# Kernel optimization log

Hardware: AMD Instinct MI355X
Metric: run time of the kernel (lower is better)

The kernel has to match this reference:

```python
import jax, jax.numpy as jnp
import numpy as np

B, C, F, H, W = 4, 256, 16, 32, 32


def setup_inputs() -> dict:
    key = jax.random.key(0)
    ks = jax.random.split(key, 8)
    x = jax.random.normal(ks[0], (B, C, F, H, W), dtype=jnp.float32)
    wq = jax.random.normal(ks[1], (C, C), dtype=jnp.float32) * 0.05
    bq = jax.random.normal(ks[2], (C,), dtype=jnp.float32) * 0.05
    wk = jax.random.normal(ks[3], (C, C), dtype=jnp.float32) * 0.05
    bk = jax.random.normal(ks[4], (C,), dtype=jnp.float32) * 0.05
    wv = jax.random.normal(ks[5], (C, C), dtype=jnp.float32) * 0.05
    bv = jax.random.normal(ks[6], (C,), dtype=jnp.float32) * 0.05
    gamma = jax.random.normal(ks[7], (1,), dtype=jnp.float32) * 0.1
    return {"x": x, "wq": wq, "bq": bq, "wk": wk, "bk": bk, "wv": wv, "bv": bv, "gamma": gamma}


def reference(x, wq, bq, wk, bk, wv, bv, gamma):
    b, c, f, h, w = x.shape
    p = h * w
    # replicate torch .view(batch*frames, channels, H, W): raw memory reinterpretation
    xr = x.reshape(b * f, c, p)  # [B*F, C, HW]
    proj = lambda wt, bi: jnp.einsum('ncp,dc->ndp', xr, wt) + bi[None, :, None]
    q = proj(wq, bq).reshape(b, f, c, p).transpose(0, 2, 1, 3)  # [B, C, F, HW]
    k = proj(wk, bk).reshape(b, f, c, p).transpose(0, 2, 3, 1)  # [B, C, HW, F]
    v = proj(wv, bv).reshape(b, f, c, p).transpose(0, 2, 1, 3)  # [B, C, F, HW]
    attn = jax.nn.softmax(jnp.matmul(q, k) * (1.0 / c ** 0.5), axis=-1)  # [B, C, F, F]
    out = jnp.matmul(attn, v)  # [B, C, F, HW]
    # replicate permute(0,2,1,3).view(B,F,C,H,W).permute(0,2,1,3,4)
    out = out.transpose(0, 2, 1, 3).reshape(b, f, c, h, w).transpose(0, 2, 1, 3, 4)
    return gamma * out + x
```

## Files before the change

kernel.cpp:

```cpp
#include <hip/hip_runtime.h>
#include <hip/hip_bf16.h>

#define CC 256
#define FF 16
#define PP 1024
#define BB 4
#define NN 64

typedef __bf16 bf16x8 __attribute__((ext_vector_type(8)));
typedef float  f32x4  __attribute__((ext_vector_type(4)));

__device__ __forceinline__ void async16(const __hip_bfloat16* g, char* l) {
    __builtin_amdgcn_global_load_lds(
        (const __attribute__((address_space(1))) unsigned int*)g,
        (__attribute__((address_space(3))) unsigned int*)l, 16, 0, 0);
}

__global__ __launch_bounds__(256) void xt_kernel(
    const float* __restrict__ x, __hip_bfloat16* __restrict__ Xt)
{
    __shared__ float T[64][65];
    const int n = blockIdx.z, c0 = blockIdx.y * 64, p0 = blockIdx.x * 64;
    const int t = threadIdx.x;
    const int pl = t & 63, r0 = t >> 6;
    const float* xp = x + ((size_t)n * CC + c0) * PP + p0;
    #pragma unroll
    for (int i = 0; i < 16; ++i) {
        const int cl = r0 + i * 4;
        T[cl][pl] = xp[(size_t)cl * PP + pl];
    }
    __syncthreads();
    __hip_bfloat16* op = Xt + ((size_t)n * PP + p0) * CC + c0;
    const int cl2 = (t & 31) * 2, q0 = t >> 5;
    #pragma unroll
    for (int j = 0; j < 8; ++j) {
        const int pr = q0 + j * 8;
        __hip_bfloat162 h;
        h.x = __float2bfloat16(T[cl2][pr]);
        h.y = __float2bfloat16(T[cl2 + 1][pr]);
        *(__hip_bfloat162*)(op + (size_t)pr * CC + cl2) = h;
    }
}

__global__ __launch_bounds__(256) void wconv_kernel(
    const float* __restrict__ wq, const float* __restrict__ wk,
    const float* __restrict__ wv, __hip_bfloat16* __restrict__ Wb)
{
    const int proj = blockIdx.y;
    const float* src = proj == 0 ? wq : (proj == 1 ? wk : wv);
    __hip_bfloat16* dst = Wb + (size_t)proj * CC * CC;
    const int idx = (blockIdx.x * 256 + threadIdx.x) * 4;
    const float4 v = *(const float4*)(src + idx);
    dst[idx + 0] = __float2bfloat16(v.x);
    dst[idx + 1] = __float2bfloat16(v.y);
    dst[idx + 2] = __float2bfloat16(v.z);
    dst[idx + 3] = __float2bfloat16(v.w);
}

__global__ __launch_bounds__(256) void qkv_mfma(
    const __hip_bfloat16* __restrict__ Wb, const __hip_bfloat16* __restrict__ Xt,
    const float* __restrict__ bq, const float* __restrict__ bk,
    const float* __restrict__ bv,
    __hip_bfloat16* __restrict__ Qw, __hip_bfloat16* __restrict__ Kw,
    float* __restrict__ Vout)
{
    __shared__ char lds[36864];

    const int p0 = blockIdx.x * 128, d0 = blockIdx.y * 128;
    const int z = blockIdx.z, proj = z % 3, n = z / 3;
    const int t = threadIdx.x, w = t >> 6, lane = t & 63;
    const int wd = (w >> 1) * 64, wp = (w & 1) * 64;
    const int q = lane >> 4, m16 = lane & 15;

    const __hip_bfloat16* Abase = Wb + (size_t)proj * CC * CC + (size_t)d0 * CC;
    const __hip_bfloat16* Bbase = Xt + (size_t)n * PP * CC + (size_t)p0 * CC;

    f32x4 acc[4][4];
    #pragma unroll
    for (int i = 0; i < 4; ++i)
        #pragma unroll
        for (int j = 0; j < 4; ++j)
            acc[i][j] = (f32x4){0.f, 0.f, 0.f, 0.f};

    for (int c0 = 0; c0 < CC; c0 += 64) {
        #pragma unroll
        for (int k = 0; k < 4; ++k) {
            const int s = t + 256 * k;
            const int row = s >> 3;
            const int gc = (s & 7) ^ (row & 7);
            async16(Abase + (size_t)row * CC + c0 + gc * 8, lds + s * 16);
            async16(Bbase + (size_t)row * CC + c0 + gc * 8, lds + 16384 + s * 16);
        }
        __syncthreads();
        #pragma unroll
        for (int kk = 0; kk < 2; ++kk) {
            bf16x8 a[4], b[4];
            #pragma unroll
            for (int i = 0; i < 4; ++i) {
                const int row = wd + i * 16 + m16;
                const int col = (4 * kk + q) ^ (row & 7);
                a[i] = *(const bf16x8*)(lds + row * 128 + col * 16);
            }
            #pragma unroll
            for (int j = 0; j < 4; ++j) {
                const int row = wp + j * 16 + m16;
                const int col = (4 * kk + q) ^ (row & 7);
                b[j] = *(const bf16x8*)(lds + 16384 + row * 128 + col * 16);
            }
            #pragma unroll
            for (int i = 0; i < 4; ++i)
                #pragma unroll
                for (int j = 0; j < 4; ++j)
                    acc[i][j] = __builtin_amdgcn_mfma_f32_16x16x32_bf16(a[i], b[j], acc[i][j], 0, 0, 0);
        }
        __syncthreads();
    }

    __syncthreads();
    char* wb = lds + w * 9216;
    const int dl2 = lane >> 3, pl2 = lane & 7;

    if (proj < 2) {
        const float* bias = (proj == 0) ? bq : bk;
        #pragma unroll
        for (int i = 0; i < 4; ++i)
            #pragma unroll
            for (int r = 0; r < 4; ++r) {
                const int d_l = i * 16 + q * 4 + r;
                const float bb = bias[d0 + wd + d_l];
                #pragma unroll
                for (int j = 0; j < 4; ++j) {
                    const int p_l = j * 16 + m16;
                    *(__hip_bfloat16*)(wb + d_l * 144 + p_l * 2) =
                        __float2bfloat16(acc[i][j][r] + bb);
                }
            }
        __hip_bfloat16* dst = ((proj == 0) ? Qw : Kw) + (size_t)n * CC * PP;
        #pragma unroll
        for (int k = 0; k < 8; ++k) {
            const int d_l = k * 8 + dl2;
            bf16x8 v = *(const bf16x8*)(wb + d_l * 144 + pl2 * 16);
            *(bf16x8*)(dst + (size_t)(d0 + wd + d_l) * PP + p0 + wp + pl2 * 8) = v;
        }
    } else {
        const int b = n >> 4, f = n & 15;
        #pragma unroll
        for (int h = 0; h < 2; ++h) {
            #pragma unroll
            for (int i = 0; i < 4; ++i)
                #pragma unroll
                for (int r = 0; r < 4; ++r) {
                    const int d_l = i * 16 + q * 4 + r;
                    const float bb = bv[d0 + wd + d_l];
                    #pragma unroll
                    for (int jj = 0; jj < 2; ++jj) {
                        const int j = 2 * h + jj;
                        const int p_rel = jj * 16 + m16;
                        *(float*)(wb + d_l * 144 + p_rel * 4) = acc[i][j][r] + bb;
                    }
                }
            #pragma unroll
            for (int k = 0; k < 8; ++k) {
                const int d_l = k * 8 + dl2;
                f32x4 v = *(const f32x4*)(wb + d_l * 144 + pl2 * 16);
                const int p = p0 + wp + h * 32 + pl2 * 4;
                *(f32x4*)(Vout + (((size_t)(b * CC + d0 + wd + d_l)) * FF + f) * PP + p) = v;
            }
        }
    }
}

__global__ __launch_bounds__(256) void attn_out(
    const __hip_bfloat16* __restrict__ Qw, const __hip_bfloat16* __restrict__ Kw,
    const float* __restrict__ x, const float* __restrict__ gamma,
    float* __restrict__ out)
{
    const int d = blockIdx.x, b = blockIdx.y;
    const int t = threadIdx.x, w = t >> 6, lane = t & 63;
    const int q = lane >> 4, m16 = lane & 15;
    __shared__ float Sp[4][16][17];
    __shared__ float As[16][17];

    {
        const size_t gbase = ((size_t)(b * 16 + m16) * CC + d) * PP + w * 256 + q * 8;
        f32x4 acc0 = {0.f, 0.f, 0.f, 0.f}, acc1 = {0.f, 0.f, 0.f, 0.f};
        #pragma unroll
        for (int pc = 0; pc < 256; pc += 64) {
            bf16x8 aq0 = *(const bf16x8*)(Qw + gbase + pc);
            bf16x8 bk0 = *(const bf16x8*)(Kw + gbase + pc);
            bf16x8 aq1 = *(const bf16x8*)(Qw + gbase + pc + 32);
            bf16x8 bk1 = *(const bf16x8*)(Kw + gbase + pc + 32);
            acc0 = __builtin_amdgcn_mfma_f32_16x16x32_bf16(aq0, bk0, acc0, 0, 0, 0);
            acc1 = __builtin_amdgcn_mfma_f32_16x16x32_bf16(aq1, bk1, acc1, 0, 0, 0);
        }
        #pragma unroll
        for (int r = 0; r < 4; ++r)
            Sp[w][q * 4 + r][m16] = acc0[r] + acc1[r];
    }
    __syncthreads();

    {
        const int f1 = t >> 4, f2 = t & 15;
        const float s = (Sp[0][f1][f2] + Sp[1][f1][f2] + Sp[2][f1][f2] + Sp[3][f1][f2]) * 0.0625f;
        float m = s;
        #pragma unroll
        for (int off = 1; off < 16; off <<= 1) m = fmaxf(m, __shfl_xor(m, off));
        const float e = __expf(s - m);
        float den = e;
        #pragma unroll
        for (int off = 1; off < 16; off <<= 1) den += __shfl_xor(den, off);
        As[f1][f2] = e / den;
    }
    __syncthreads();

    const float g = gamma[0];
    const size_t base = ((size_t)(b * CC + d) * FF) * PP + t * 4;
    f32x4 vv[16];
    #pragma unroll
    for (int f2 = 0; f2 < 16; ++f2)
        vv[f2] = *(const f32x4*)(out + base + (size_t)f2 * PP);
    #pragma unroll
    for (int f1 = 0; f1 < 16; ++f1) {
        f32x4 a = {0.f, 0.f, 0.f, 0.f};
        #pragma unroll
        for (int f2 = 0; f2 < 16; ++f2) {
            const float av = As[f1][f2];
            a += av * vv[f2];
        }
        const f32x4 xv = *(const f32x4*)(x + base + (size_t)f1 * PP);
        const f32x4 res = g * a + xv;
        *(f32x4*)(out + base + (size_t)f1 * PP) = res;
    }
}

extern "C" void kernel_launch(void* const* d_in, const int* in_sizes, int n_in,
                              void* d_out, int out_size, void* d_ws, size_t ws_size,
                              hipStream_t stream) {
    const float* x     = (const float*)d_in[0];
    const float* wq    = (const float*)d_in[1];
    const float* bq    = (const float*)d_in[2];
    const float* wk    = (const float*)d_in[3];
    const float* bk    = (const float*)d_in[4];
    const float* wv    = (const float*)d_in[5];
    const float* bv    = (const float*)d_in[6];
    const float* gamma = (const float*)d_in[7];
    float* out = (float*)d_out;

    __hip_bfloat16* Qw = (__hip_bfloat16*)d_ws;
    __hip_bfloat16* Kw = Qw + (size_t)NN * CC * PP;
    __hip_bfloat16* Xt = Kw + (size_t)NN * CC * PP;
    __hip_bfloat16* Wb = Xt + (size_t)NN * CC * PP;

    wconv_kernel<<<dim3(CC * CC / (256 * 4), 3), 256, 0, stream>>>(wq, wk, wv, Wb);
    xt_kernel<<<dim3(PP / 64, CC / 64, NN), 256, 0, stream>>>(x, Xt);
    qkv_mfma<<<dim3(PP / 128, CC / 128, NN * 3), 256, 0, stream>>>(
        Wb, Xt, bq, bk, bv, Qw, Kw, out);
    attn_out<<<dim3(CC, BB), 256, 0, stream>>>(Qw, Kw, x, gamma, out);
}
```

Baseline: 200.7 us.

## Store V in bf16 workspace, fuse weight conversion into transpose kernel

V projection output is written as bf16 to a dedicated workspace buffer instead of fp32 into the output tensor, and attn_out reads and widens it. This halves V write and read traffic. The weight-conversion kernel is folded into xt_kernel as an extra z-slice, removing one launch. Xt is now staged in the output buffer. Storing V in bf16 adds rounding error to the attention output.

```diff
diff --git a/kernel.cpp b/kernel.cpp
--- a/kernel.cpp
+++ b/kernel.cpp
@@ -16,12 +16,38 @@
         (__attribute__((address_space(3))) unsigned int*)l, 16, 0, 0);
 }
 
+__device__ __forceinline__ float bf2f(unsigned short u) {
+    union { unsigned i; float f; } v; v.i = ((unsigned)u) << 16; return v.f;
+}
+
 __global__ __launch_bounds__(256) void xt_kernel(
-    const float* __restrict__ x, __hip_bfloat16* __restrict__ Xt)
+    const float* __restrict__ x,
+    const float* __restrict__ wq, const float* __restrict__ wk,
+    const float* __restrict__ wv,
+    __hip_bfloat16* __restrict__ Xt, __hip_bfloat16* __restrict__ Wb)
 {
     __shared__ float T[64][65];
-    const int n = blockIdx.z, c0 = blockIdx.y * 64, p0 = blockIdx.x * 64;
+    const int n = blockIdx.z;
     const int t = threadIdx.x;
+
+    if (n == NN) {
+        const int blk = blockIdx.y * 16 + blockIdx.x;
+        const int idx = (blk * 256 + t) * 4;
+        #pragma unroll
+        for (int proj = 0; proj < 3; ++proj) {
+            const float* src = proj == 0 ? wq : (proj == 1 ? wk : wv);
+            __hip_bfloat16* dst = Wb + (size_t)proj * CC * CC;
+            const float4 v = *(const float4*)(src + idx);
+            __hip_bfloat162 h0, h1;
+            h0.x = __float2bfloat16(v.x); h0.y = __float2bfloat16(v.y);
+            h1.x = __float2bfloat16(v.z); h1.y = __float2bfloat16(v.w);
+            *(__hip_bfloat162*)(dst + idx)     = h0;
+            *(__hip_bfloat162*)(dst + idx + 2) = h1;
+        }
+        return;
+    }
+
+    const int c0 = blockIdx.y * 64, p0 = blockIdx.x * 64;
     const int pl = t & 63, r0 = t >> 6;
     const float* xp = x + ((size_t)n * CC + c0) * PP + p0;
     #pragma unroll
@@ -42,27 +68,12 @@
     }
 }
 
-__global__ __launch_bounds__(256) void wconv_kernel(
-    const float* __restrict__ wq, const float* __restrict__ wk,
-    const float* __restrict__ wv, __hip_bfloat16* __restrict__ Wb)
-{
-    const int proj = blockIdx.y;
-    const float* src = proj == 0 ? wq : (proj == 1 ? wk : wv);
-    __hip_bfloat16* dst = Wb + (size_t)proj * CC * CC;
-    const int idx = (blockIdx.x * 256 + threadIdx.x) * 4;
-    const float4 v = *(const float4*)(src + idx);
-    dst[idx + 0] = __float2bfloat16(v.x);
-    dst[idx + 1] = __float2bfloat16(v.y);
-    dst[idx + 2] = __float2bfloat16(v.z);
-    dst[idx + 3] = __float2bfloat16(v.w);
-}
-
 __global__ __launch_bounds__(256) void qkv_mfma(
     const __hip_bfloat16* __restrict__ Wb, const __hip_bfloat16* __restrict__ Xt,
     const float* __restrict__ bq, const float* __restrict__ bk,
     const float* __restrict__ bv,
     __hip_bfloat16* __restrict__ Qw, __hip_bfloat16* __restrict__ Kw,
-    float* __restrict__ Vout)
+    __hip_bfloat16* __restrict__ Vw)
 {
     __shared__ char lds[36864];
 
@@ -120,58 +131,43 @@
     char* wb = lds + w * 9216;
     const int dl2 = lane >> 3, pl2 = lane & 7;
 
+    const float* bias = (proj == 0) ? bq : ((proj == 1) ? bk : bv);
+    #pragma unroll
+    for (int i = 0; i < 4; ++i)
+        #pragma unroll
+        for (int r = 0; r < 4; ++r) {
+            const int d_l = i * 16 + q * 4 + r;
+            const float bb = bias[d0 + wd + d_l];
+            #pragma unroll
+            for (int j = 0; j < 4; ++j) {
+                const int p_l = j * 16 + m16;
+                *(__hip_bfloat16*)(wb + d_l * 144 + p_l * 2) =
+                    __float2bfloat16(acc[i][j][r] + bb);
+            }
+        }
+
+    __hip_bfloat16* dst;
+    size_t dstride;
     if (proj < 2) {
-        const float* bias = (proj == 0) ? bq : bk;
-        #pragma unroll
-        for (int i = 0; i < 4; ++i)
-            #pragma unroll
-            for (int r = 0; r < 4; ++r) {
-                const int d_l = i * 16 + q * 4 + r;
-                const float bb = bias[d0 + wd + d_l];
-                #pragma unroll
-                for (int j = 0; j < 4; ++j) {
-                    const int p_l = j * 16 + m16;
-                    *(__hip_bfloat16*)(wb + d_l * 144 + p_l * 2) =
-                        __float2bfloat16(acc[i][j][r] + bb);
-                }
-            }
-        __hip_bfloat16* dst = ((proj == 0) ? Qw : Kw) + (size_t)n * CC * PP;
-        #pragma unroll
-        for (int k = 0; k < 8; ++k) {
-            const int d_l = k * 8 + dl2;
-            bf16x8 v = *(const bf16x8*)(wb + d_l * 144 + pl2 * 16);
-            *(bf16x8*)(dst + (size_t)(d0 + wd + d_l) * PP + p0 + wp + pl2 * 8) = v;
-        }
+        dst = ((proj == 0) ? Qw : Kw) + (size_t)n * CC * PP
+              + (size_t)(d0 + wd) * PP + p0 + wp;
+        dstride = PP;
     } else {
         const int b = n >> 4, f = n & 15;
-        #pragma unroll
-        for (int h = 0; h < 2; ++h) {
-            #pragma unroll
-            for (int i = 0; i < 4; ++i)
-                #pragma unroll
-                for (int r = 0; r < 4; ++r) {
-                    const int d_l = i * 16 + q * 4 + r;
-                    const float bb = bv[d0 + wd + d_l];
-                    #pragma unroll
-                    for (int jj = 0; jj < 2; ++jj) {
-                        const int j = 2 * h + jj;
-                        const int p_rel = jj * 16 + m16;
-                        *(float*)(wb + d_l * 144 + p_rel * 4) = acc[i][j][r] + bb;
-                    }
-                }
-            #pragma unroll
-            for (int k = 0; k < 8; ++k) {
-                const int d_l = k * 8 + dl2;
-                f32x4 v = *(const f32x4*)(wb + d_l * 144 + pl2 * 16);
-                const int p = p0 + wp + h * 32 + pl2 * 4;
-                *(f32x4*)(Vout + (((size_t)(b * CC + d0 + wd + d_l)) * FF + f) * PP + p) = v;
-            }
-        }
+        dst = Vw + (((size_t)(b * CC + d0 + wd)) * FF + f) * PP + p0 + wp;
+        dstride = (size_t)FF * PP;
+    }
+    #pragma unroll
+    for (int k = 0; k < 8; ++k) {
+        const int d_l = k * 8 + dl2;
+        bf16x8 v = *(const bf16x8*)(wb + d_l * 144 + pl2 * 16);
+        *(bf16x8*)(dst + (size_t)d_l * dstride + pl2 * 8) = v;
     }
 }
 
 __global__ __launch_bounds__(256) void attn_out(
     const __hip_bfloat16* __restrict__ Qw, const __hip_bfloat16* __restrict__ Kw,
+    const __hip_bfloat16* __restrict__ Vw,
     const float* __restrict__ x, const float* __restrict__ gamma,
     float* __restrict__ out)
 {
@@ -215,10 +211,13 @@
 
     const float g = gamma[0];
     const size_t base = ((size_t)(b * CC + d) * FF) * PP + t * 4;
+    const __hip_bfloat16* Vb = Vw + base;
     f32x4 vv[16];
     #pragma unroll
-    for (int f2 = 0; f2 < 16; ++f2)
-        vv[f2] = *(const f32x4*)(out + base + (size_t)f2 * PP);
+    for (int f2 = 0; f2 < 16; ++f2) {
+        const ushort4 rv = *(const ushort4*)(Vb + (size_t)f2 * PP);
+        vv[f2] = (f32x4){ bf2f(rv.x), bf2f(rv.y), bf2f(rv.z), bf2f(rv.w) };
+    }
     #pragma unroll
     for (int f1 = 0; f1 < 16; ++f1) {
         f32x4 a = {0.f, 0.f, 0.f, 0.f};
@@ -248,12 +247,13 @@
 
     __hip_bfloat16* Qw = (__hip_bfloat16*)d_ws;
     __hip_bfloat16* Kw = Qw + (size_t)NN * CC * PP;
-    __hip_bfloat16* Xt = Kw + (size_t)NN * CC * PP;
-    __hip_bfloat16* Wb = Xt + (size_t)NN * CC * PP;
-
-    wconv_kernel<<<dim3(CC * CC / (256 * 4), 3), 256, 0, stream>>>(wq, wk, wv, Wb);
-    xt_kernel<<<dim3(PP / 64, CC / 64, NN), 256, 0, stream>>>(x, Xt);
+    __hip_bfloat16* Vw = Kw + (size_t)NN * CC * PP;
+    __hip_bfloat16* Wb = Vw + (size_t)NN * CC * PP;
+    __hip_bfloat16* Xt = (__hip_bfloat16*)d_out;
+
+    xt_kernel<<<dim3(PP / 64, CC / 64, NN + 1), 256, 0, stream>>>(
+        x, wq, wk, wv, Xt, Wb);
     qkv_mfma<<<dim3(PP / 128, CC / 128, NN * 3), 256, 0, stream>>>(
-        Wb, Xt, bq, bk, bv, Qw, Kw, out);
-    attn_out<<<dim3(CC, BB), 256, 0, stream>>>(Qw, Kw, x, gamma, out);
-}
+        Wb, Xt, bq, bk, bv, Qw, Kw, Vw);
+    attn_out<<<dim3(CC, BB), 256, 0, stream>>>(Qw, Kw, Vw, x, gamma, out);
+}
```

New measurement: 192.5 us. 4.0% less time.
